# Kernel optimization log

Measured on AMD Instinct MI355X. Metric: run time of the kernel, lower is better.

## Reference

```python
import jax, jax.numpy as jnp
import numpy as np
import math

N_HEADS = 16

def _rope_tables(T, D, dtype):
    # inv_freq over even dims, emb = [freqs, freqs] -> [T, D]
    inv_freq = 1.0 / (10000.0 ** (jnp.arange(0, D, 2, dtype=jnp.float32) / D))
    freqs = jnp.arange(T, dtype=jnp.float32)[:, None] * inv_freq[None, :]  # [T, D/2]
    emb = jnp.concatenate([freqs, freqs], axis=-1)  # [T, D]
    return jnp.cos(emb).astype(dtype), jnp.sin(emb).astype(dtype)

def _rotate_half(x):
    d = x.shape[-1] // 2
    return jnp.concatenate([-x[..., d:], x[..., :d]], axis=-1)

def setup_inputs() -> dict:
    key = jax.random.key(0)
    ks = jax.random.split(key, 5)
    B, T, C = 2, 2048, 1024
    s = 1.0 / math.sqrt(C)
    return {
        "x": jax.random.normal(ks[0], (B, T, C), dtype=jnp.float32),
        "Wq": jax.random.normal(ks[1], (C, C), dtype=jnp.float32) * s,
        "Wk": jax.random.normal(ks[2], (C, C), dtype=jnp.float32) * s,
        "Wv": jax.random.normal(ks[3], (C, C), dtype=jnp.float32) * s,
        "Wo": jax.random.normal(ks[4], (C, C), dtype=jnp.float32) * s,
    }

def reference(x, Wq, Wk, Wv, Wo):
    B, T, C = x.shape
    H = N_HEADS
    D = C // H
    # QKV projections (torch Linear, bias=False: y = x @ W.T), split into heads
    def proj(W):
        return (x @ W.T).reshape(B, T, H, D).transpose(0, 2, 1, 3)  # [B,H,T,D]
    q, k, v = proj(Wq), proj(Wk), proj(Wv)
    # RoPE
    cos, sin = _rope_tables(T, D, x.dtype)  # [T,D] each, broadcast over B,H
    q = q * cos + _rotate_half(q) * sin
    k = k * cos + _rotate_half(k) * sin
    # scaled dot-product attention with causal mask
    scale = 1.0 / math.sqrt(D)
    attn = jnp.einsum('bhtd,bhsd->bhts', q, k) * scale  # [B,H,T,T]
    row = jnp.arange(T)[:, None]
    col = jnp.arange(T)[None, :]
    attn = jnp.where(col > row, -jnp.inf, attn)
    p = jax.nn.softmax(attn, axis=-1)
    out = jnp.einsum('bhts,bhsd->bhtd', p, v)  # [B,H,T,D]
    out = out.transpose(0, 2, 1, 3).reshape(B, T, C)
    return out @ Wo.T
```

## Files before the change

### kernel.cpp

```cpp
#include <hip/hip_runtime.h>
#include <hip/hip_bf16.h>


typedef __hip_bfloat16 bf16;
typedef __attribute__((ext_vector_type(8))) short bf16x8;
typedef __attribute__((ext_vector_type(4))) float f32x4;
typedef __attribute__((ext_vector_type(4))) short short4v;

#define MFMA16(a, b, c) __builtin_amdgcn_mfma_f32_16x16x32_bf16((a), (b), (c), 0, 0, 0)

constexpr int Bn = 2, Hn = 16, Tn = 2048, Dn = 64, Cn = 1024;
constexpr size_t NE = (size_t)Bn * Tn * Cn;
constexpr size_t WE = (size_t)Cn * Cn;
constexpr float QSCALE = 0.125f * 1.44269504088896f;

__device__ inline unsigned short bfbits(float x) {
    bf16 b = __float2bfloat16(x);
    return *(unsigned short*)&b;
}

__device__ inline bf16x8 pack8(f32x4 a, f32x4 b) {
    bf16x8 r;
#pragma unroll
    for (int i = 0; i < 4; ++i) r[i] = (short)bfbits(a[i]);
#pragma unroll
    for (int i = 0; i < 4; ++i) r[4 + i] = (short)bfbits(b[i]);
    return r;
}

__device__ inline void gl_lds16(const bf16* g, unsigned short* l) {
    __builtin_amdgcn_global_load_lds(
        (const __attribute__((address_space(1))) void*)g,
        (__attribute__((address_space(3))) void*)l, 16, 0, 0);
}

__device__ inline void stage128(const bf16* gbase, int ld, unsigned short* lds,
                                int wave, int lane) {
#pragma unroll
    for (int j = 0; j < 4; ++j) {
        int p = j * 256 + wave * 64 + lane;
        int row = p >> 3, ch = (p & 7) ^ (row & 7);
        gl_lds16(gbase + (size_t)row * ld + ch * 8,
                 lds + (size_t)(j * 256 + wave * 64) * 8);
    }
}
__device__ inline void stage64(const bf16* gbase, int ld, unsigned short* lds,
                               int wave, int lane) {
#pragma unroll
    for (int j = 0; j < 2; ++j) {
        int p = j * 256 + wave * 64 + lane;
        int row = p >> 3, ch = (p & 7) ^ (row & 7);
        gl_lds16(gbase + (size_t)row * ld + ch * 8,
                 lds + (size_t)(j * 256 + wave * 64) * 8);
    }
}

__device__ inline bf16x8 ldsfrag(const unsigned short* base, int row, int ch) {
    return *(const bf16x8*)&base[row * 64 + ((ch ^ (row & 7)) * 8)];
}

__global__ __launch_bounds__(256) void convert_kernel(
    const float* __restrict__ x, const float* __restrict__ wq,
    const float* __restrict__ wk, const float* __restrict__ wv,
    const float* __restrict__ wo, bf16* __restrict__ dst)
{
    int blk = blockIdx.x;
    int lane = threadIdx.x & 63;
    int lx = lane & 15, quad = lane >> 4;
    const float* src;
    size_t doff;
    if (blk < 2048) {
        int frag = blk * 4 + (threadIdx.x >> 6);
        int mt = frag >> 5, kc = frag & 31;
        src = x + (size_t)(mt * 16 + lx) * Cn + kc * 32 + quad * 8;
        doff = (size_t)frag * 512 + lane * 8;
    } else {
        int w = (blk - 2048) >> 9, b = (blk - 2048) & 511;
        const float* s4[4] = {wq, wk, wv, wo};
        int frag = b * 4 + (threadIdx.x >> 6);
        int nb = frag >> 5, kc = frag & 31;
        src = s4[w] + (size_t)(nb * 16 + lx) * Cn + kc * 32 + quad * 8;
        doff = NE + (size_t)w * WE + (size_t)frag * 512 + lane * 8;
    }
    f32x4 a = *(const f32x4*)(src);
    f32x4 b2 = *(const f32x4*)(src + 4);
    *(bf16x8*)(dst + doff) = pack8(a, b2);
}

__global__ __launch_bounds__(256) void gemm_qkv_kernel(
    const bf16* __restrict__ Xf, const bf16* __restrict__ Wbase,
    bf16* __restrict__ Qo, bf16* __restrict__ Ko, bf16* __restrict__ Vo)
{
    const int bm = blockIdx.x, bn = blockIdx.y, wsel = blockIdx.z;
    const bf16* W = Wbase + (size_t)wsel * WE;
    const int tid  = threadIdx.x;
    const int wave = tid >> 6, lane = tid & 63;
    const int lx   = lane & 15, quad = lane >> 4;
    const int wm = wave >> 1, wn = wave & 1;

    const int mt0 = bm * 8 + wm * 4;
    const int nb0 = bn * 8 + wn * 4;
    const bf16* afrag = Xf + (size_t)mt0 * 32 * 512 + (size_t)lane * 8;
    const bf16* wfrag = W + (size_t)nb0 * 32 * 512 + (size_t)lane * 8;

    f32x4 acc[4][4] = {};
    bf16x8 acur[4], bcur[4], anxt[4], bnxt[4];
#pragma unroll
    for (int i = 0; i < 4; ++i) {
        acur[i] = *(const bf16x8*)(afrag + (size_t)i * 32 * 512);
        bcur[i] = *(const bf16x8*)(wfrag + (size_t)i * 32 * 512);
    }
    for (int kc = 0; kc < 32; ++kc) {
        if (kc < 31) {
#pragma unroll
            for (int i = 0; i < 4; ++i) {
                anxt[i] = *(const bf16x8*)(afrag + ((size_t)i * 32 + kc + 1) * 512);
                bnxt[i] = *(const bf16x8*)(wfrag + ((size_t)i * 32 + kc + 1) * 512);
            }
        }
#pragma unroll
        for (int mt = 0; mt < 4; ++mt)
#pragma unroll
            for (int nt = 0; nt < 4; ++nt)
                acc[mt][nt] = MFMA16(acur[mt], bcur[nt], acc[mt][nt]);
#pragma unroll
        for (int i = 0; i < 4; ++i) { acur[i] = anxt[i]; bcur[i] = bnxt[i]; }
    }

    const int h = bn * 2 + wn;
    if (wsel <= 1) {
#pragma unroll
        for (int mt = 0; mt < 4; ++mt)
#pragma unroll
            for (int r = 0; r < 4; ++r) {
                int mg = bm * 128 + wm * 64 + mt * 16 + quad * 4 + r;
                int t  = mg & (Tn - 1);
#pragma unroll
                for (int nt = 0; nt < 2; ++nt) {
                    int d = nt * 16 + lx;
                    float ang = (float)t * __expf(-(float)d * 0.2878231366f);
                    float c, s;
                    __sincosf(ang, &s, &c);
                    float a0 = acc[mt][nt][r], a1 = acc[mt][nt + 2][r];
                    acc[mt][nt][r]     = a0 * c - a1 * s;
                    acc[mt][nt + 2][r] = a1 * c + a0 * s;
                }
            }
    }

#pragma unroll
    for (int mt = 0; mt < 4; ++mt) {
        int mg0 = bm * 128 + wm * 64 + mt * 16 + quad * 4;
        int b = mg0 >> 11, t0 = mg0 & (Tn - 1);
        if (wsel == 0) {
#pragma unroll
            for (int nt = 0; nt < 4; ++nt)
#pragma unroll
                for (int r = 0; r < 4; ++r) {
                    int d = nt * 16 + lx;
                    Qo[((size_t)(b * Hn + h) * Tn + t0 + r) * Dn + d] =
                        __float2bfloat16(acc[mt][nt][r] * QSCALE);
                }
        } else if (wsel == 1) {
#pragma unroll
            for (int nt = 0; nt < 4; ++nt)
#pragma unroll
                for (int r = 0; r < 4; ++r) {
                    int d = nt * 16 + lx;
                    Ko[((size_t)(b * Hn + h) * Tn + t0 + r) * Dn + d] =
                        __float2bfloat16(acc[mt][nt][r]);
                }
        } else {
#pragma unroll
            for (int nt = 0; nt < 4; ++nt) {
                int d = nt * 16 + lx;
                short4v pk;
#pragma unroll
                for (int r = 0; r < 4; ++r) pk[r] = (short)bfbits(acc[mt][nt][r]);
                *(short4v*)&Vo[((size_t)(b * Hn + h) * Dn + d) * Tn + t0] = pk;
            }
        }
    }
}

__global__ __launch_bounds__(256) void gemm_out_kernel(
    const bf16* __restrict__ A, const bf16* __restrict__ W, float* __restrict__ Out)
{
    __shared__ unsigned short As[128 * 64];
    const int bm = blockIdx.x, bn = blockIdx.y;
    const int tid  = threadIdx.x;
    const int wave = tid >> 6, lane = tid & 63;
    const int lx   = lane & 15, quad = lane >> 4;
    const int wm = wave >> 1, wn = wave & 1;

    const bf16* abase = A + (size_t)(bm * 128) * Cn;
    const int nb0 = bn * 4 + wn * 2;
    const bf16* wfrag = W + (size_t)nb0 * 32 * 512 + (size_t)lane * 8;

    f32x4 acc[4][2] = {};
    for (int kt = 0; kt < Cn / 64; ++kt) {
        __syncthreads();
        stage128(abase + kt * 64, Cn, As, wave, lane);
        bf16x8 bfv[2][2];
#pragma unroll
        for (int nt = 0; nt < 2; ++nt)
#pragma unroll
            for (int ks = 0; ks < 2; ++ks)
                bfv[nt][ks] = *(const bf16x8*)(wfrag +
                    ((size_t)nt * 32 + kt * 2 + ks) * 512);
        __syncthreads();
#pragma unroll
        for (int ks = 0; ks < 2; ++ks) {
            bf16x8 af[4];
#pragma unroll
            for (int mt = 0; mt < 4; ++mt)
                af[mt] = ldsfrag(As, wm * 64 + mt * 16 + lx, ks * 4 + quad);
#pragma unroll
            for (int mt = 0; mt < 4; ++mt)
#pragma unroll
                for (int nt = 0; nt < 2; ++nt)
                    acc[mt][nt] = MFMA16(af[mt], bfv[nt][ks], acc[mt][nt]);
        }
    }
#pragma unroll
    for (int mt = 0; mt < 4; ++mt)
#pragma unroll
        for (int nt = 0; nt < 2; ++nt)
#pragma unroll
            for (int r = 0; r < 4; ++r) {
                int mg = bm * 128 + wm * 64 + mt * 16 + quad * 4 + r;
                int ng = bn * 64 + wn * 32 + nt * 16 + lx;
                Out[(size_t)mg * Cn + ng] = acc[mt][nt][r];
            }
}

__global__ __launch_bounds__(256) void attn_kernel(
    const bf16* __restrict__ Q, const bf16* __restrict__ K,
    const bf16* __restrict__ Vt, bf16* __restrict__ O)
{
    __shared__ unsigned short Ks[64 * 64];
    __shared__ unsigned short Vs[64 * 64];
    __shared__ unsigned short Pl[4][16 * 72];
    const int f  = blockIdx.x;
    const int bh = (f & 7) * 4 + ((f >> 3) & 3);
    const int qb = 31 - (f >> 5);
    const int tid  = threadIdx.x;
    const int wave = tid >> 6, lane = tid & 63;
    const int lx   = lane & 15, quad = lane >> 4;

    const bf16* Qh = Q  + (size_t)bh * Tn * Dn;
    const bf16* Kh = K  + (size_t)bh * Tn * Dn;
    const bf16* Vh = Vt + (size_t)bh * Dn * Tn;
    unsigned short* pw = &Pl[wave][0];

    const int qrowA = qb * 64 + wave * 16 + lx;
    bf16x8 aq0 = *(const bf16x8*)(Qh + (size_t)qrowA * Dn + quad * 8);
    bf16x8 aq1 = *(const bf16x8*)(Qh + (size_t)qrowA * Dn + 32 + quad * 8);

    bf16x8 ones;
#pragma unroll
    for (int i = 0; i < 8; ++i) ones[i] = (short)0x3F80;

    f32x4 acc_o[4] = {};
    f32x4 acc_l = {};
    const int row_local = wave * 16 + quad * 4;

    for (int c = 0; c <= qb; ++c) {
        __syncthreads();
        stage64(Kh + (size_t)c * 64 * Dn, Dn, Ks, wave, lane);
        stage64(Vh + (size_t)c * 64, Tn, Vs, wave, lane);
        __syncthreads();
        f32x4 accs[4] = {};
#pragma unroll
        for (int nt = 0; nt < 4; ++nt) {
            int key = nt * 16 + lx;
            bf16x8 k0 = ldsfrag(Ks, key, quad);
            bf16x8 k1 = ldsfrag(Ks, key, quad + 4);
            accs[nt] = MFMA16(aq0, k0, accs[nt]);
            accs[nt] = MFMA16(aq1, k1, accs[nt]);
        }
        if (c < qb) {
#pragma unroll
            for (int nt = 0; nt < 4; ++nt)
#pragma unroll
                for (int r = 0; r < 4; ++r)
                    pw[(quad * 4 + r) * 72 + nt * 16 + lx] = bfbits(exp2f(accs[nt][r]));
        } else {
#pragma unroll
            for (int nt = 0; nt < 4; ++nt) {
                int keyl = nt * 16 + lx;
#pragma unroll
                for (int r = 0; r < 4; ++r) {
                    float p = (keyl > row_local + r) ? 0.0f : exp2f(accs[nt][r]);
                    pw[(quad * 4 + r) * 72 + nt * 16 + lx] = bfbits(p);
                }
            }
        }
        asm volatile("s_waitcnt lgkmcnt(0)" ::: "memory");
        bf16x8 ap0 = *(const bf16x8*)&pw[lx * 72 + quad * 8];
        bf16x8 ap1 = *(const bf16x8*)&pw[lx * 72 + 32 + quad * 8];
        acc_l = MFMA16(ap0, ones, acc_l);
        acc_l = MFMA16(ap1, ones, acc_l);
#pragma unroll
        for (int dt = 0; dt < 4; ++dt) {
            int d = dt * 16 + lx;
            bf16x8 v0 = ldsfrag(Vs, d, quad);
            bf16x8 v1 = ldsfrag(Vs, d, quad + 4);
            acc_o[dt] = MFMA16(ap0, v0, acc_o[dt]);
            acc_o[dt] = MFMA16(ap1, v1, acc_o[dt]);
        }
    }

    const int b = bh >> 4, h = bh & 15;
#pragma unroll
    for (int dt = 0; dt < 4; ++dt)
#pragma unroll
        for (int r = 0; r < 4; ++r) {
            int t = qb * 64 + row_local + r;
            int d = dt * 16 + lx;
            float o = acc_o[dt][r] / acc_l[r];
            O[((size_t)(b * Tn + t) * Hn + h) * Dn + d] = __float2bfloat16(o);
        }
}

extern "C" void kernel_launch(void* const* d_in, const int* in_sizes, int n_in,
                              void* d_out, int out_size, void* d_ws, size_t ws_size,
                              hipStream_t stream)
{
    const float* x  = (const float*)d_in[0];
    const float* Wq = (const float*)d_in[1];
    const float* Wk = (const float*)d_in[2];
    const float* Wv = (const float*)d_in[3];
    const float* Wo = (const float*)d_in[4];
    float* out = (float*)d_out;

    bf16* ws = (bf16*)d_ws;
    bf16* Xf = ws;
    bf16* Wb = ws + NE;
    bf16* Qb = ws + NE + 4 * WE;
    bf16* Kb = Qb + NE;
    bf16* Vb = Kb + NE;
    bf16* Ab = Xf;

    convert_kernel<<<4096, 256, 0, stream>>>(x, Wq, Wk, Wv, Wo, ws);
    gemm_qkv_kernel<<<dim3(32, 8, 3), 256, 0, stream>>>(Xf, Wb, Qb, Kb, Vb);
    attn_kernel<<<1024, 256, 0, stream>>>(Qb, Kb, Vb, Ab);
    gemm_out_kernel<<<dim3(32, 16), 256, 0, stream>>>(Ab, Wb + 3 * WE, out);
}
```

Baseline: 177.2 us.

## Write attention output in MFMA fragment layout and drop LDS staging in out-proj

The attention kernel now stores its output directly in a pre-swizzled MFMA A-fragment layout instead of row-major [B,T,C]. The output-projection GEMM can then load A fragments straight from global memory into registers, with register double-buffering, instead of staging through LDS with two barriers per k-step. This removes the LDS traffic and synchronization in the out-projection. In exchange the attention epilogue does scattered 2-byte stores, and the GEMM relies on global-load latency being hidden by the one-step prefetch.

```diff
diff --git a/kernel.cpp b/kernel.cpp
--- a/kernel.cpp
+++ b/kernel.cpp
@@ -34,16 +34,6 @@
         (__attribute__((address_space(3))) void*)l, 16, 0, 0);
 }
 
-__device__ inline void stage128(const bf16* gbase, int ld, unsigned short* lds,
-                                int wave, int lane) {
-#pragma unroll
-    for (int j = 0; j < 4; ++j) {
-        int p = j * 256 + wave * 64 + lane;
-        int row = p >> 3, ch = (p & 7) ^ (row & 7);
-        gl_lds16(gbase + (size_t)row * ld + ch * 8,
-                 lds + (size_t)(j * 256 + wave * 64) * 8);
-    }
-}
 __device__ inline void stage64(const bf16* gbase, int ld, unsigned short* lds,
                                int wave, int lane) {
 #pragma unroll
@@ -184,43 +174,45 @@
 }
 
 __global__ __launch_bounds__(256) void gemm_out_kernel(
-    const bf16* __restrict__ A, const bf16* __restrict__ W, float* __restrict__ Out)
-{
-    __shared__ unsigned short As[128 * 64];
+    const bf16* __restrict__ Af, const bf16* __restrict__ W, float* __restrict__ Out)
+{
     const int bm = blockIdx.x, bn = blockIdx.y;
     const int tid  = threadIdx.x;
     const int wave = tid >> 6, lane = tid & 63;
     const int lx   = lane & 15, quad = lane >> 4;
     const int wm = wave >> 1, wn = wave & 1;
 
-    const bf16* abase = A + (size_t)(bm * 128) * Cn;
+    const int mt0 = bm * 8 + wm * 4;
     const int nb0 = bn * 4 + wn * 2;
+    const bf16* afrag = Af + (size_t)mt0 * 32 * 512 + (size_t)lane * 8;
     const bf16* wfrag = W + (size_t)nb0 * 32 * 512 + (size_t)lane * 8;
 
     f32x4 acc[4][2] = {};
-    for (int kt = 0; kt < Cn / 64; ++kt) {
-        __syncthreads();
-        stage128(abase + kt * 64, Cn, As, wave, lane);
-        bf16x8 bfv[2][2];
-#pragma unroll
-        for (int nt = 0; nt < 2; ++nt)
-#pragma unroll
-            for (int ks = 0; ks < 2; ++ks)
-                bfv[nt][ks] = *(const bf16x8*)(wfrag +
-                    ((size_t)nt * 32 + kt * 2 + ks) * 512);
-        __syncthreads();
-#pragma unroll
-        for (int ks = 0; ks < 2; ++ks) {
-            bf16x8 af[4];
-#pragma unroll
-            for (int mt = 0; mt < 4; ++mt)
-                af[mt] = ldsfrag(As, wm * 64 + mt * 16 + lx, ks * 4 + quad);
-#pragma unroll
-            for (int mt = 0; mt < 4; ++mt)
-#pragma unroll
-                for (int nt = 0; nt < 2; ++nt)
-                    acc[mt][nt] = MFMA16(af[mt], bfv[nt][ks], acc[mt][nt]);
-        }
+    bf16x8 acur[4], bcur[2], anxt[4], bnxt[2];
+#pragma unroll
+    for (int i = 0; i < 4; ++i)
+        acur[i] = *(const bf16x8*)(afrag + (size_t)i * 32 * 512);
+#pragma unroll
+    for (int i = 0; i < 2; ++i)
+        bcur[i] = *(const bf16x8*)(wfrag + (size_t)i * 32 * 512);
+    for (int kc = 0; kc < 32; ++kc) {
+        if (kc < 31) {
+#pragma unroll
+            for (int i = 0; i < 4; ++i)
+                anxt[i] = *(const bf16x8*)(afrag + ((size_t)i * 32 + kc + 1) * 512);
+#pragma unroll
+            for (int i = 0; i < 2; ++i)
+                bnxt[i] = *(const bf16x8*)(wfrag + ((size_t)i * 32 + kc + 1) * 512);
+        }
+#pragma unroll
+        for (int mt = 0; mt < 4; ++mt)
+#pragma unroll
+            for (int nt = 0; nt < 2; ++nt)
+                acc[mt][nt] = MFMA16(acur[mt], bcur[nt], acc[mt][nt]);
+#pragma unroll
+        for (int i = 0; i < 4; ++i) acur[i] = anxt[i];
+#pragma unroll
+        for (int i = 0; i < 2; ++i) bcur[i] = bnxt[i];
     }
 #pragma unroll
     for (int mt = 0; mt < 4; ++mt)
@@ -312,15 +304,18 @@
     }
 
     const int b = bh >> 4, h = bh & 15;
-#pragma unroll
-    for (int dt = 0; dt < 4; ++dt)
+    const int mtile = b * 128 + qb * 4 + wave;
+#pragma unroll
+    for (int dt = 0; dt < 4; ++dt) {
+        int ch = h * 64 + dt * 16 + lx;
+        size_t base = ((size_t)mtile * 32 + (ch >> 5)) * 512
+                    + (size_t)(((ch >> 3) & 3) * 16) * 8 + (ch & 7);
 #pragma unroll
         for (int r = 0; r < 4; ++r) {
-            int t = qb * 64 + row_local + r;
-            int d = dt * 16 + lx;
             float o = acc_o[dt][r] / acc_l[r];
-            O[((size_t)(b * Tn + t) * Hn + h) * Dn + d] = __float2bfloat16(o);
-        }
+            O[base + (size_t)(quad * 4 + r) * 8] = __float2bfloat16(o);
+        }
+    }
 }
 
 extern "C" void kernel_launch(void* const* d_in, const int* in_sizes, int n_in,
```

After: 176.2 us. About the same (-0.6%).
